# Kernel tuning notes

Hardware: AMD Instinct MI355X
Metric: run time of the kernel (lower is better)

The kernel has to match this reference:

```python
import jax, jax.numpy as jnp
import numpy as np


def setup_inputs() -> dict:
    key = jax.random.key(0)
    ks = jax.random.split(key, 8)
    N, E, F, H = 50000, 400000, 128, 512
    x = jax.random.normal(ks[0], (N, F), dtype=jnp.float32)
    edge_index = jax.random.randint(ks[1], (2, E), 0, N, dtype=jnp.int32)
    W1 = jax.random.normal(ks[2], (H, 2 * F), dtype=jnp.float32) * 0.05
    b1 = jax.random.normal(ks[3], (H,), dtype=jnp.float32) * 0.05
    W2 = jax.random.normal(ks[4], (H, 2 * H), dtype=jnp.float32) * 0.05
    b2 = jax.random.normal(ks[5], (H,), dtype=jnp.float32) * 0.05
    Wo = jax.random.normal(ks[6], (1, H), dtype=jnp.float32) * 0.05
    bo = jax.random.normal(ks[7], (1,), dtype=jnp.float32) * 0.05
    return {"x": x, "edge_index": edge_index, "W1": W1, "b1": b1,
            "W2": W2, "b2": b2, "Wo": Wo, "bo": bo}


def reference(x, edge_index, W1, b1, W2, b2, Wo, bo):
    # GraphSAGE mean aggregation: agg[dst] = mean over incoming edges of h[src]
    N = x.shape[0]
    src = edge_index[0]
    dst = edge_index[1]
    deg = jax.ops.segment_sum(jnp.ones_like(dst, dtype=x.dtype), dst,
                              num_segments=N)
    inv_deg = 1.0 / jnp.maximum(deg, 1.0)  # clamp_min(1.0)

    def agg_mean(h):
        s = jax.ops.segment_sum(h[src], dst, num_segments=N)  # [N, D]
        return s * inv_deg[:, None]

    # Layer 1: concat(self, neigh) -> Linear -> ReLU (dropout = identity, eval)
    n1 = agg_mean(x)
    h1 = jax.nn.relu(jnp.concatenate([x, n1], axis=1) @ W1.T + b1)
    # Layer 2
    n2 = agg_mean(h1)
    h2 = jax.nn.relu(jnp.concatenate([h1, n2], axis=1) @ W2.T + b2)
    # Output head
    logits = h2 @ Wo.T + bo  # [N, 1]
    return jax.nn.sigmoid(logits)
```

## Files before the change

kernel.cpp:

```cpp
#include <hip/hip_runtime.h>
#include <math.h>


typedef __attribute__((ext_vector_type(8))) short bf16x8;
typedef __attribute__((ext_vector_type(4))) float f32x4;

static inline int ceil_div(int a, int b) { return (a + b - 1) / b; }

__device__ inline float bf2f_lo(unsigned u) { return __builtin_bit_cast(float, u << 16); }
__device__ inline float bf2f_hi(unsigned u) { return __builtin_bit_cast(float, u & 0xffff0000u); }
__device__ inline unsigned f2bf(float f) {
    unsigned u = __builtin_bit_cast(unsigned, f);
    u += 0x7fffu + ((u >> 16) & 1u);
    return u >> 16;
}

#define GLOAD_LDS16(gp, lp)                                                   \
    __builtin_amdgcn_global_load_lds(                                         \
        (__attribute__((address_space(1))) void*)(gp),                        \
        (__attribute__((address_space(3))) void*)(lp), 16, 0, 0)


__global__ void cvt3_hist_kernel(const float* __restrict__ a, unsigned short* __restrict__ ao, int na4,
                                 const float* __restrict__ b, unsigned short* __restrict__ bo, int nb4,
                                 const float* __restrict__ c, unsigned short* __restrict__ co, int nc4,
                                 const int* __restrict__ dst, int* __restrict__ deg, int E,
                                 int cvt_blocks) {
    if ((int)blockIdx.x < cvt_blocks) {
        int i = blockIdx.x * 256 + threadIdx.x;
        if (i < na4 + nb4) {
            const float* in; unsigned short* out; int k;
            if (i < na4) { in = a; out = ao; k = i; }
            else         { in = b; out = bo; k = i - na4; }
            float4 v = ((const float4*)in)[k];
            ushort4 o;
            o.x = (unsigned short)f2bf(v.x);
            o.y = (unsigned short)f2bf(v.y);
            o.z = (unsigned short)f2bf(v.z);
            o.w = (unsigned short)f2bf(v.w);
            ((ushort4*)out)[k] = o;
        } else if (i < na4 + nb4 + nc4) {
            int kk = i - na4 - nb4;
            float4 v = ((const float4*)c)[kk];
            ushort4 o;
            o.x = (unsigned short)f2bf(v.x);
            o.y = (unsigned short)f2bf(v.y);
            o.z = (unsigned short)f2bf(v.z);
            o.w = (unsigned short)f2bf(v.w);
            const int cc = kk >> 8;
            const int kq = kk & 255;
            const int t    = kq >> 3;
            const int quad = (kq >> 1) & 3;
            const int j0   = (kq & 1) * 4;
            const int g  = cc >> 6, nt = (cc >> 4) & 3, cl = cc & 15;
            const size_t off =
                ((((size_t)(t * 8 + g) * 4 + nt) * 4 + quad) * 16 + cl) * 8 + j0;
            *(ushort4*)(co + off) = o;
        }
    } else {
        int e = (blockIdx.x - cvt_blocks) * 256 + threadIdx.x;
        if (e < E) atomicAdd(&deg[dst[e]], 1);
    }
}


__global__ __launch_bounds__(256) void chunk_reduce(const int* __restrict__ deg,
                                                    int* __restrict__ partial, int N) {
    int base = blockIdx.x * 1024;
    int s = 0;
    for (int i = threadIdx.x; i < 1024; i += 256) {
        int idx = base + i;
        if (idx < N) s += deg[idx];
    }
    #pragma unroll
    for (int off = 32; off; off >>= 1) s += __shfl_down(s, off);
    __shared__ int ws[4];
    if ((threadIdx.x & 63) == 0) ws[threadIdx.x >> 6] = s;
    __syncthreads();
    if (threadIdx.x == 0) partial[blockIdx.x] = ws[0] + ws[1] + ws[2] + ws[3];
}

__global__ void partial_scan(int* __restrict__ partial, int* __restrict__ rowstartN, int P) {
    int lane = threadIdx.x;
    int v = (lane < P) ? partial[lane] : 0;
    int incl = v;
    #pragma unroll
    for (int off = 1; off < 64; off <<= 1) {
        int t = __shfl_up(incl, off);
        if (lane >= off) incl += t;
    }
    if (lane < P) partial[lane] = incl - v;
    if (lane == 63) *rowstartN = incl;
}

__global__ __launch_bounds__(256) void chunk_scan(const int* __restrict__ deg,
                                                  const int* __restrict__ partial,
                                                  int* __restrict__ rowstart,
                                                  int* __restrict__ cursor, int N) {
    int base = blockIdx.x * 1024 + threadIdx.x * 4;
    int v[4];
    #pragma unroll
    for (int j = 0; j < 4; ++j) {
        int i = base + j;
        v[j] = (i < N) ? deg[i] : 0;
    }
    int mysum = v[0] + v[1] + v[2] + v[3];
    int incl = mysum;
    int lane = threadIdx.x & 63, wave = threadIdx.x >> 6;
    #pragma unroll
    for (int off = 1; off < 64; off <<= 1) {
        int t = __shfl_up(incl, off);
        if (lane >= off) incl += t;
    }
    __shared__ int ws[4];
    if (lane == 63) ws[wave] = incl;
    __syncthreads();
    int run = partial[blockIdx.x] + incl - mysum;
    for (int w = 0; w < wave; ++w) run += ws[w];
    #pragma unroll
    for (int j = 0; j < 4; ++j) {
        int i = base + j;
        if (i < N) { rowstart[i] = run; cursor[i] = run; }
        run += v[j];
    }
}

__global__ void bucket_kernel(const int* __restrict__ src, const int* __restrict__ dst,
                              int* __restrict__ cursor, int* __restrict__ ebuf, int E) {
    int e = blockIdx.x * 256 + threadIdx.x;
    if (e < E) {
        int pos = atomicAdd(&cursor[dst[e]], 1);
        ebuf[pos] = src[e];
    }
}


__global__ void gather_mean_128(const int* __restrict__ rowstart, const int* __restrict__ ebuf,
                                const unsigned* __restrict__ featb, unsigned* __restrict__ outb, int N) {
    int w = (blockIdx.x * blockDim.x + threadIdx.x) >> 6;
    int lane = threadIdx.x & 63;
    if (w >= N) return;
    int e0 = rowstart[w], e1 = rowstart[w + 1];
    float ax = 0.0f, ay = 0.0f;
    for (int i = e0; i < e1; i += 8) {
        int idx[8];
        #pragma unroll
        for (int u = 0; u < 8; ++u) {
            int t = i + u;
            idx[u] = ebuf[t < e1 ? t : e1 - 1];
        }
        unsigned v[8];
        #pragma unroll
        for (int u = 0; u < 8; ++u)
            v[u] = featb[(size_t)idx[u] * 64 + lane];
        #pragma unroll
        for (int u = 0; u < 8; ++u) {
            const float s = (i + u < e1) ? 1.0f : 0.0f;
            ax += s * bf2f_lo(v[u]);
            ay += s * bf2f_hi(v[u]);
        }
    }
    float inv = 1.0f / fmaxf((float)(e1 - e0), 1.0f);
    outb[(size_t)w * 64 + lane] = f2bf(ax * inv) | (f2bf(ay * inv) << 16);
}

__global__ void gather_mean_512(const int* __restrict__ rowstart, const int* __restrict__ ebuf,
                                const unsigned short* __restrict__ featb,
                                unsigned short* __restrict__ outb, int N) {
    int w = (blockIdx.x * blockDim.x + threadIdx.x) >> 6;
    int lane = threadIdx.x & 63;
    if (w >= N) return;
    int e0 = rowstart[w], e1 = rowstart[w + 1];
    float a[8] = {0, 0, 0, 0, 0, 0, 0, 0};
    const uint4* base = (const uint4*)featb;
    for (int i = e0; i < e1; i += 8) {
        int idx[8];
        #pragma unroll
        for (int u = 0; u < 8; ++u) {
            int t = i + u;
            idx[u] = ebuf[t < e1 ? t : e1 - 1];
        }
        uint4 v[8];
        #pragma unroll
        for (int u = 0; u < 8; ++u)
            v[u] = base[(size_t)idx[u] * 64 + lane];
        #pragma unroll
        for (int u = 0; u < 8; ++u) {
            const float s = (i + u < e1) ? 1.0f : 0.0f;
            a[0] += s * bf2f_lo(v[u].x); a[1] += s * bf2f_hi(v[u].x);
            a[2] += s * bf2f_lo(v[u].y); a[3] += s * bf2f_hi(v[u].y);
            a[4] += s * bf2f_lo(v[u].z); a[5] += s * bf2f_hi(v[u].z);
            a[6] += s * bf2f_lo(v[u].w); a[7] += s * bf2f_hi(v[u].w);
        }
    }
    float inv = 1.0f / fmaxf((float)(e1 - e0), 1.0f);
    uint4 o;
    o.x = f2bf(a[0] * inv) | (f2bf(a[1] * inv) << 16);
    o.y = f2bf(a[2] * inv) | (f2bf(a[3] * inv) << 16);
    o.z = f2bf(a[4] * inv) | (f2bf(a[5] * inv) << 16);
    o.w = f2bf(a[6] * inv) | (f2bf(a[7] * inv) << 16);
    ((uint4*)outb)[(size_t)w * 64 + lane] = o;
}

__global__ __launch_bounds__(256) void gemm_mfma(
    const unsigned short* __restrict__ A0,
    const unsigned short* __restrict__ A1,
    const unsigned short* __restrict__ W,
    const float* __restrict__ b,
    unsigned short* __restrict__ outb,
    const float* __restrict__ Wo,
    float* __restrict__ logit,
    int N, int K0, int K1, int C, int mode)
{
    const int nrow = (N + 127) >> 7;
    const int id   = blockIdx.x;
    const int rowb = ((id >> 5) << 3) + (id & 7);
    const int colb = (id >> 3) & 3;
    if (rowb >= nrow) return;

    const int K = K0 + K1;
    const int S = K0;
    __shared__ short As[2][4096];
    __shared__ short Bs[2][4096];

    const int tid  = threadIdx.x;
    const int lane = tid & 63;
    const int wave = tid >> 6;
    const int wm = wave & 1, wn = wave >> 1;
    const int cl = lane & 15, quad = lane >> 4;
    const int row0 = rowb * 128;
    const int col0 = colb * 128;

    const int r = lane >> 2;
    const int j = lane & 3;
    const int trow0 = wave * 32 + r;
    const int trow1 = trow0 + 16;
    const int ar0 = (row0 + trow0 < N) ? row0 + trow0 : N - 1;
    const int ar1 = (row0 + trow1 < N) ? row0 + trow1 : N - 1;
    const size_t aoff0 = (size_t)ar0 * S + j * 8;
    const size_t aoff1 = (size_t)ar1 * S + j * 8;
    const size_t boff0 = (size_t)(col0 + trow0) * K + j * 8;
    const size_t boff1 = (size_t)(col0 + trow1) * K + j * 8;
    const int lds0 = (wave * 32) * 32;
    const int lds1 = (wave * 32 + 16) * 32;

    f32x4 acc[4][4];
    #pragma unroll
    for (int mt = 0; mt < 4; ++mt)
        #pragma unroll
        for (int nt = 0; nt < 4; ++nt)
            acc[mt][nt] = (f32x4){0.f, 0.f, 0.f, 0.f};

    GLOAD_LDS16(A0 + aoff0, &As[0][lds0]);
    GLOAD_LDS16(A0 + aoff1, &As[0][lds1]);
    GLOAD_LDS16(W  + boff0, &Bs[0][lds0]);
    GLOAD_LDS16(W  + boff1, &Bs[0][lds1]);

    const int iters = K >> 5;
    for (int i = 0; i < iters; ++i) {
        const int cur = i & 1;
        __syncthreads();
        if (i + 1 < iters) {
            const int kn = (i + 1) << 5;
            const unsigned short* Ab = (kn < K0) ? (A0 + kn) : (A1 + (kn - K0));
            const unsigned short* Wb = W + kn;
            const int nb = cur ^ 1;
            GLOAD_LDS16(Ab + aoff0, &As[nb][lds0]);
            GLOAD_LDS16(Ab + aoff1, &As[nb][lds1]);
            GLOAD_LDS16(Wb + boff0, &Bs[nb][lds0]);
            GLOAD_LDS16(Wb + boff1, &Bs[nb][lds1]);
        }

        bf16x8 af[4], bfr[4];
        #pragma unroll
        for (int mt = 0; mt < 4; ++mt)
            af[mt] = *(const bf16x8*)&As[cur][(wm * 64 + mt * 16 + cl) * 32 + quad * 8];
        #pragma unroll
        for (int nt = 0; nt < 4; ++nt)
            bfr[nt] = *(const bf16x8*)&Bs[cur][(wn * 64 + nt * 16 + cl) * 32 + quad * 8];

        #pragma unroll
        for (int mt = 0; mt < 4; ++mt)
            #pragma unroll
            for (int nt = 0; nt < 4; ++nt)
                acc[mt][nt] = __builtin_amdgcn_mfma_f32_16x16x32_bf16(
                    af[mt], bfr[nt], acc[mt][nt], 0, 0, 0);
    }

    if (mode == 0) {
        #pragma unroll
        for (int nt = 0; nt < 4; ++nt) {
            const int colx = col0 + wn * 64 + nt * 16 + cl;
            const float bb = b[colx];
            #pragma unroll
            for (int mt = 0; mt < 4; ++mt) {
                #pragma unroll
                for (int rr = 0; rr < 4; ++rr) {
                    int row = row0 + wm * 64 + mt * 16 + quad * 4 + rr;
                    if (row < N)
                        outb[(size_t)row * C + colx] =
                            (unsigned short)f2bf(fmaxf(acc[mt][nt][rr] + bb, 0.0f));
                }
            }
        }
    } else {
        float bv[4], wv2[4];
        #pragma unroll
        for (int nt = 0; nt < 4; ++nt) {
            const int colx = col0 + wn * 64 + nt * 16 + cl;
            bv[nt] = b[colx];
            wv2[nt] = Wo[colx];
        }
        #pragma unroll
        for (int mt = 0; mt < 4; ++mt) {
            #pragma unroll
            for (int rr = 0; rr < 4; ++rr) {
                float s = 0.0f;
                #pragma unroll
                for (int nt = 0; nt < 4; ++nt)
                    s += fmaxf(acc[mt][nt][rr] + bv[nt], 0.0f) * wv2[nt];
                s += __shfl_xor(s, 1);
                s += __shfl_xor(s, 2);
                s += __shfl_xor(s, 4);
                s += __shfl_xor(s, 8);
                int row = row0 + wm * 64 + mt * 16 + quad * 4 + rr;
                if (cl == 0 && row < N) atomicAdd(&logit[row], s);
            }
        }
    }
}


#define STGA(kt) do {                                                          \
    const unsigned short* _p = ((kt) < 16) ? (A0 + ((kt) << 5))                \
                                           : (A1 + (((kt) - 16) << 5));        \
    GLOAD_LDS16(_p + offA, lds + ((kt) % 3) * 8192 + w * 1024);                \
} while (0)

#define LDB(kt) do {                                                           \
    _Pragma("unroll")                                                          \
    for (int _n = 0; _n < 4; ++_n)                                             \
        bq[_n] = *(const bf16x8*)(W +                                          \
            (((size_t)(kt) * 8 + gB) * 4 + _n) * 512 + l * 8);                 \
} while (0)

#define RDA(bf) do {                                                           \
    _Pragma("unroll")                                                          \
    for (int _m = 0; _m < 4; ++_m)                                             \
        af[_m] = *(const bf16x8*)(lds + (bf) * 8192 + aoff + _m * 1024);       \
} while (0)

#define MM16B() do {                                                           \
    _Pragma("unroll")                                                          \
    for (int _m = 0; _m < 4; ++_m)                                             \
        _Pragma("unroll")                                                      \
        for (int _n = 0; _n < 4; ++_n)                                         \
            acc[_m][_n] = __builtin_amdgcn_mfma_f32_16x16x32_bf16(             \
                af[_m], bq[_n], acc[_m][_n], 0, 0, 0);                         \
} while (0)

#define PHASE4(t, stage) do {                                                  \
    __builtin_amdgcn_sched_barrier(0);                                         \
    asm volatile("s_waitcnt vmcnt(5)" ::: "memory");                           \
    __builtin_amdgcn_s_barrier();                                              \
    __builtin_amdgcn_sched_barrier(0);                                         \
    RDA((t) % 3);                                                              \
    if (stage) STGA((t) + 2);                                                  \
    __builtin_amdgcn_s_setprio(1);                                             \
    MM16B();                                                                   \
    __builtin_amdgcn_s_setprio(0);                                             \
    if ((t) + 1 < 32) LDB((t) + 1);                                            \
} while (0)

__global__ __launch_bounds__(512, 4) void gemm2_breg(
    const unsigned short* __restrict__ A0,
    const unsigned short* __restrict__ A1,
    const unsigned short* __restrict__ W,
    const float* __restrict__ b,
    const float* __restrict__ Wo,
    float* __restrict__ logit,
    int N)
{
    __shared__ char lds[24576];

    const int nwg  = ((N + 127) >> 7) * 2;
    const int orig = blockIdx.x;
    const int xcd = orig & 7, lnum = orig >> 3;
    const int q = nwg >> 3, r = nwg & 7;
    const int virt = (xcd < r ? xcd * (q + 1) : r * (q + 1) + (xcd - r) * q) + lnum;
    const int row0 = (virt >> 1) << 7;
    const int col0 = (virt & 1) << 8;

    const int tid = threadIdx.x;
    const int w = tid >> 6, l = tid & 63;
    const int wr = w >> 2, wc = w & 3;
    const int cl = l & 15, quad = l >> 4;
    const int gB = (col0 >> 6) + wc;

    const int c_log = (((l & 3) ^ ((l >> 3) & 3))) * 8;
    int ra = row0 + w * 16 + (l >> 2);
    if (ra > N - 1) ra = N - 1;
    const size_t offA = (size_t)ra * 512 + c_log;

    const int swz  = ((cl >> 1) & 3) << 4;
    const int aoff = (((wr * 64 + cl) * 64) + quad * 16) ^ swz;

    f32x4 acc[4][4];
    #pragma unroll
    for (int mt = 0; mt < 4; ++mt)
        #pragma unroll
        for (int nt = 0; nt < 4; ++nt)
            acc[mt][nt] = (f32x4){0.f, 0.f, 0.f, 0.f};

    bf16x8 af[4], bq[4];

    STGA(0); STGA(1);
    LDB(0);

    #pragma unroll
    for (int t = 0; t < 30; ++t)
        PHASE4(t, 1);
    PHASE4(30, 0);
    PHASE4(31, 0);
    asm volatile("s_waitcnt vmcnt(0)" ::: "memory");

    float bv[4], wv[4];
    #pragma unroll
    for (int nt = 0; nt < 4; ++nt) {
        const int colx = col0 + wc * 64 + nt * 16 + cl;
        bv[nt] = b[colx];
        wv[nt] = Wo[colx];
    }
    #pragma unroll
    for (int mt = 0; mt < 4; ++mt) {
        #pragma unroll
        for (int rr = 0; rr < 4; ++rr) {
            float s = 0.0f;
            #pragma unroll
            for (int nt = 0; nt < 4; ++nt)
                s += fmaxf(acc[mt][nt][rr] + bv[nt], 0.0f) * wv[nt];
            s += __shfl_xor(s, 1);
            s += __shfl_xor(s, 2);
            s += __shfl_xor(s, 4);
            s += __shfl_xor(s, 8);
            const int row = row0 + wr * 64 + mt * 16 + quad * 4 + rr;
            if (cl == 0 && row < N) atomicAdd(&logit[row], s);
        }
    }
}

__global__ void head_kernel(const float* __restrict__ logit, const float* __restrict__ bo,
                            float* __restrict__ out, int N) {
    int i = blockIdx.x * 256 + threadIdx.x;
    if (i < N) out[i] = 1.0f / (1.0f + expf(-(logit[i] + bo[0])));
}

extern "C" void kernel_launch(void* const* d_in, const int* in_sizes, int n_in,
                              void* d_out, int out_size, void* d_ws, size_t ws_size,
                              hipStream_t stream) {
    const float* x  = (const float*)d_in[0];
    const int*   ei = (const int*)d_in[1];
    const float* W1 = (const float*)d_in[2];
    const float* b1 = (const float*)d_in[3];
    const float* W2 = (const float*)d_in[4];
    const float* b2 = (const float*)d_in[5];
    const float* Wo = (const float*)d_in[6];
    const float* bo = (const float*)d_in[7];
    float* out = (float*)d_out;

    const int N = in_sizes[0] / 128;
    const int E = in_sizes[1] / 2;
    const int* src = ei;
    const int* dst = ei + E;

    char* ws = (char*)d_ws;
    size_t off = 0;
    auto alloc = [&](size_t bytes) {
        void* p = ws + off;
        off += (bytes + 255) & ~(size_t)255;
        return p;
    };
    int* deg      = (int*)alloc((size_t)N * 4);
    int* rowstart = (int*)alloc((size_t)(N + 1) * 4);
    int* cursor   = (int*)alloc((size_t)N * 4);
    int* partial  = (int*)alloc((size_t)64 * 4);
    int* ebuf     = (int*)alloc((size_t)E * 4);
    float* logit  = (float*)alloc((size_t)N * 4);
    unsigned short* xb  = (unsigned short*)alloc((size_t)N * 128 * 2);
    unsigned short* W1b = (unsigned short*)alloc((size_t)512 * 256 * 2);
    unsigned short* W2b = (unsigned short*)alloc((size_t)512 * 1024 * 2);
    unsigned short* n1b = (unsigned short*)alloc((size_t)N * 128 * 2);
    unsigned short* h1b = (unsigned short*)alloc((size_t)N * 512 * 2);
    unsigned short* n2b = (unsigned short*)alloc((size_t)N * 512 * 2);
    (void)ws_size; (void)n_in; (void)out_size;

    hipMemsetAsync(deg,   0, (size_t)N * 4, stream);
    hipMemsetAsync(logit, 0, (size_t)N * 4, stream);

    const int na4 = N * 128 / 4, nb4 = 512 * 256 / 4, nc4 = 512 * 1024 / 4;
    const int cvt_blocks  = ceil_div(na4 + nb4 + nc4, 256);
    const int hist_blocks = ceil_div(E, 256);
    cvt3_hist_kernel<<<cvt_blocks + hist_blocks, 256, 0, stream>>>(
        x, xb, na4, W1, W1b, nb4, W2, W2b, nc4, dst, deg, E, cvt_blocks);

    const int P = ceil_div(N, 1024);
    chunk_reduce<<<P, 256, 0, stream>>>(deg, partial, N);
    partial_scan<<<1, 64, 0, stream>>>(partial, rowstart + N, P);
    chunk_scan<<<P, 256, 0, stream>>>(deg, partial, rowstart, cursor, N);
    bucket_kernel<<<ceil_div(E, 256), 256, 0, stream>>>(src, dst, cursor, ebuf, E);

    const int nrow = ceil_div(N, 128);
    const int gblocks = ceil_div(nrow, 8) * 8 * 4;
    gather_mean_128<<<ceil_div(N * 64, 256), 256, 0, stream>>>(rowstart, ebuf,
                                                               (const unsigned*)xb, (unsigned*)n1b, N);
    gemm_mfma<<<gblocks, 256, 0, stream>>>(xb, n1b, W1b, b1, h1b, nullptr, nullptr,
                                           N, 128, 128, 512, 0);

    gather_mean_512<<<ceil_div(N * 64, 256), 256, 0, stream>>>(rowstart, ebuf, h1b, n2b, N);
    const int g2 = ceil_div(N, 128) * 2;
    gemm2_breg<<<g2, 512, 0, stream>>>(h1b, n2b, W2b, b2, Wo, logit, N);

    head_kernel<<<ceil_div(N, 256), 256, 0, stream>>>(logit, bo, out, N);
}
```

Baseline: 317.1 us.

## Make layer-2 GEMM barrier-free with per-wave private A staging and double-buffered B

Replaces the 512-thread, 128x256-tile layer-2 GEMM with a 256-thread, 64x256-tile kernel. In it each wave stages its own full copy of the A tile into a private LDS slice, so the per-step workgroup barrier goes away and only vmcnt waits remain. B fragments are now double-buffered in two register sets to hide global load latency. The cost is that every wave loads A redundantly (4x A traffic and LDS use), there are twice as many workgroups, and register pressure rises under the new launch bounds.

Result: slower. 333.2 us (+5.1%).

```diff
diff --git a/kernel.cpp b/kernel.cpp
--- a/kernel.cpp
+++ b/kernel.cpp
@@ -331,48 +331,44 @@
 }
 
 
-#define STGA(kt) do {                                                          \
+#define STGA2(kt, _bf) do {                                                    \
     const unsigned short* _p = ((kt) < 16) ? (A0 + ((kt) << 5))                \
                                            : (A1 + (((kt) - 16) << 5));        \
-    GLOAD_LDS16(_p + offA, lds + ((kt) % 3) * 8192 + w * 1024);                \
+    GLOAD_LDS16(_p + offA[0], myl + (_bf) * 4096);                             \
+    GLOAD_LDS16(_p + offA[1], myl + (_bf) * 4096 + 1024);                      \
+    GLOAD_LDS16(_p + offA[2], myl + (_bf) * 4096 + 2048);                      \
+    GLOAD_LDS16(_p + offA[3], myl + (_bf) * 4096 + 3072);                      \
 } while (0)
 
-#define LDB(kt) do {                                                           \
+#define LDB2(kt, bqr) do {                                                     \
     _Pragma("unroll")                                                          \
     for (int _n = 0; _n < 4; ++_n)                                             \
-        bq[_n] = *(const bf16x8*)(W +                                          \
+        bqr[_n] = *(const bf16x8*)(W +                                         \
             (((size_t)(kt) * 8 + gB) * 4 + _n) * 512 + l * 8);                 \
 } while (0)
 
-#define RDA(bf) do {                                                           \
+#define RDA2(_bf) do {                                                         \
     _Pragma("unroll")                                                          \
     for (int _m = 0; _m < 4; ++_m)                                             \
-        af[_m] = *(const bf16x8*)(lds + (bf) * 8192 + aoff + _m * 1024);       \
+        af[_m] = *(const bf16x8*)(myl + (_bf) * 4096 + aoff + _m * 1024);      \
 } while (0)
 
-#define MM16B() do {                                                           \
+#define MM16W(bqr) do {                                                        \
     _Pragma("unroll")                                                          \
     for (int _m = 0; _m < 4; ++_m)                                             \
         _Pragma("unroll")                                                      \
         for (int _n = 0; _n < 4; ++_n)                                         \
             acc[_m][_n] = __builtin_amdgcn_mfma_f32_16x16x32_bf16(             \
-                af[_m], bq[_n], acc[_m][_n], 0, 0, 0);                         \
+                af[_m], bqr[_n], acc[_m][_n], 0, 0, 0);                        \
 } while (0)
 
-#define PHASE4(t, stage) do {                                                  \
+#define GATE(nstr) do {                                                        \
     __builtin_amdgcn_sched_barrier(0);                                         \
-    asm volatile("s_waitcnt vmcnt(5)" ::: "memory");                           \
-    __builtin_amdgcn_s_barrier();                                              \
+    asm volatile("s_waitcnt vmcnt(" nstr ")" ::: "memory");                    \
     __builtin_amdgcn_sched_barrier(0);                                         \
-    RDA((t) % 3);                                                              \
-    if (stage) STGA((t) + 2);                                                  \
-    __builtin_amdgcn_s_setprio(1);                                             \
-    MM16B();                                                                   \
-    __builtin_amdgcn_s_setprio(0);                                             \
-    if ((t) + 1 < 32) LDB((t) + 1);                                            \
 } while (0)
 
-__global__ __launch_bounds__(512, 4) void gemm2_breg(
+__global__ __launch_bounds__(256, 3) void gemm2_wnb(
     const unsigned short* __restrict__ A0,
     const unsigned short* __restrict__ A1,
     const unsigned short* __restrict__ W,
@@ -381,29 +377,33 @@
     float* __restrict__ logit,
     int N)
 {
-    __shared__ char lds[24576];
-
-    const int nwg  = ((N + 127) >> 7) * 2;
+    __shared__ char lds[49152];
+
+    const int nwg  = ((N + 63) >> 6) * 2;
     const int orig = blockIdx.x;
     const int xcd = orig & 7, lnum = orig >> 3;
     const int q = nwg >> 3, r = nwg & 7;
     const int virt = (xcd < r ? xcd * (q + 1) : r * (q + 1) + (xcd - r) * q) + lnum;
-    const int row0 = (virt >> 1) << 7;
+    const int row0 = (virt >> 1) << 6;
     const int col0 = (virt & 1) << 8;
 
     const int tid = threadIdx.x;
     const int w = tid >> 6, l = tid & 63;
-    const int wr = w >> 2, wc = w & 3;
     const int cl = l & 15, quad = l >> 4;
-    const int gB = (col0 >> 6) + wc;
+    const int gB = (col0 >> 6) + w;
+    char* myl = lds + w * 12288;
 
     const int c_log = (((l & 3) ^ ((l >> 3) & 3))) * 8;
-    int ra = row0 + w * 16 + (l >> 2);
-    if (ra > N - 1) ra = N - 1;
-    const size_t offA = (size_t)ra * 512 + c_log;
+    size_t offA[4];
+    #pragma unroll
+    for (int i = 0; i < 4; ++i) {
+        int ra = row0 + i * 16 + (l >> 2);
+        if (ra > N - 1) ra = N - 1;
+        offA[i] = (size_t)ra * 512 + c_log;
+    }
 
     const int swz  = ((cl >> 1) & 3) << 4;
-    const int aoff = (((wr * 64 + cl) * 64) + quad * 16) ^ swz;
+    const int aoff = (cl * 64 + quad * 16) ^ swz;
 
     f32x4 acc[4][4];
     #pragma unroll
@@ -412,22 +412,35 @@
         for (int nt = 0; nt < 4; ++nt)
             acc[mt][nt] = (f32x4){0.f, 0.f, 0.f, 0.f};
 
-    bf16x8 af[4], bq[4];
-
-    STGA(0); STGA(1);
-    LDB(0);
-
-    #pragma unroll
-    for (int t = 0; t < 30; ++t)
-        PHASE4(t, 1);
-    PHASE4(30, 0);
-    PHASE4(31, 0);
-    asm volatile("s_waitcnt vmcnt(0)" ::: "memory");
+    bf16x8 af[4], bqA[4], bqB[4];
+
+    STGA2(0, 0); LDB2(0, bqA);
+    STGA2(1, 1); LDB2(1, bqB);
+
+    #pragma unroll
+    for (int t = 0; t < 30; t += 2) {
+        GATE("8");
+        RDA2(t % 3);
+        MM16W(bqA);
+        LDB2(t + 2, bqA);
+        STGA2(t + 2, (t + 2) % 3);
+        GATE("8");
+        RDA2((t + 1) % 3);
+        MM16W(bqB);
+        LDB2(t + 3, bqB);
+        STGA2(t + 3, (t + 3) % 3);
+    }
+    GATE("8");
+    RDA2(0);
+    MM16W(bqA);
+    GATE("0");
+    RDA2(1);
+    MM16W(bqB);
 
     float bv[4], wv[4];
     #pragma unroll
     for (int nt = 0; nt < 4; ++nt) {
-        const int colx = col0 + wc * 64 + nt * 16 + cl;
+        const int colx = col0 + w * 64 + nt * 16 + cl;
         bv[nt] = b[colx];
         wv[nt] = Wo[colx];
     }
@@ -443,7 +456,7 @@
             s += __shfl_xor(s, 2);
             s += __shfl_xor(s, 4);
             s += __shfl_xor(s, 8);
-            const int row = row0 + wr * 64 + mt * 16 + quad * 4 + rr;
+            const int row = row0 + mt * 16 + quad * 4 + rr;
             if (cl == 0 && row < N) atomicAdd(&logit[row], s);
         }
     }
@@ -517,8 +530,8 @@
                                            N, 128, 128, 512, 0);
 
     gather_mean_512<<<ceil_div(N * 64, 256), 256, 0, stream>>>(rowstart, ebuf, h1b, n2b, N);
-    const int g2 = ceil_div(N, 128) * 2;
-    gemm2_breg<<<g2, 512, 0, stream>>>(h1b, n2b, W2b, b2, Wo, logit, N);
+    const int g2 = ceil_div(N, 64) * 2;
+    gemm2_wnb<<<g2, 256, 0, stream>>>(h1b, n2b, W2b, b2, Wo, logit, N);
 
     head_kernel<<<ceil_div(N, 256), 256, 0, stream>>>(logit, bo, out, N);
 }
```

## Port layer-1 GEMM to register-resident B pipeline with pre-swizzled W1

Applied to the files above, without the earlier changes.

Replaces the generic LDS double-buffered layer-1 GEMM with a 512-thread kernel modeled on the layer-2 kernel. It streams A through a triple-buffered LDS ring, loads B directly into registers from a pre-swizzled W1 layout, and uses XCD-aware block remapping. The W1 conversion now writes the MFMA-friendly tiled layout, and B fragments are double-buffered in registers (bqA/bqB) to prefetch two k-steps ahead in both GEMMs. This aims to cut LDS traffic and barrier stalls in GEMM1, at the cost of extra register pressure and a short 8-step pipeline.

New measurement: 316.4 us. No clear change (-0.2%).

```diff
diff --git a/kernel.cpp b/kernel.cpp
--- a/kernel.cpp
+++ b/kernel.cpp
@@ -28,17 +28,31 @@
                                  int cvt_blocks) {
     if ((int)blockIdx.x < cvt_blocks) {
         int i = blockIdx.x * 256 + threadIdx.x;
-        if (i < na4 + nb4) {
-            const float* in; unsigned short* out; int k;
-            if (i < na4) { in = a; out = ao; k = i; }
-            else         { in = b; out = bo; k = i - na4; }
-            float4 v = ((const float4*)in)[k];
+        if (i < na4) {
+            float4 v = ((const float4*)a)[i];
             ushort4 o;
             o.x = (unsigned short)f2bf(v.x);
             o.y = (unsigned short)f2bf(v.y);
             o.z = (unsigned short)f2bf(v.z);
             o.w = (unsigned short)f2bf(v.w);
-            ((ushort4*)out)[k] = o;
+            ((ushort4*)ao)[i] = o;
+        } else if (i < na4 + nb4) {
+            int kk = i - na4;
+            float4 v = ((const float4*)b)[kk];
+            ushort4 o;
+            o.x = (unsigned short)f2bf(v.x);
+            o.y = (unsigned short)f2bf(v.y);
+            o.z = (unsigned short)f2bf(v.z);
+            o.w = (unsigned short)f2bf(v.w);
+            const int cc = kk >> 6;
+            const int kq = kk & 63;
+            const int t    = kq >> 3;
+            const int quad = (kq >> 1) & 3;
+            const int j0   = (kq & 1) * 4;
+            const int g  = cc >> 6, nt = (cc >> 4) & 3, cl = cc & 15;
+            const size_t off =
+                ((((size_t)(t * 8 + g) * 4 + nt) * 4 + quad) * 16 + cl) * 8 + j0;
+            *(ushort4*)(bo + off) = o;
         } else if (i < na4 + nb4 + nc4) {
             int kk = i - na4 - nb4;
             float4 v = ((const float4*)c)[kk];
@@ -202,175 +216,115 @@
     ((uint4*)outb)[(size_t)w * 64 + lane] = o;
 }
 
-__global__ __launch_bounds__(256) void gemm_mfma(
+
+#define STGAg(kt, SPL, STR) do {                                               \
+    const unsigned short* _p = ((kt) < (SPL)) ? (A0 + ((kt) << 5))             \
+                                              : (A1 + (((kt) - (SPL)) << 5));  \
+    GLOAD_LDS16(_p + offA, lds + ((kt) % 3) * 8192 + w * 1024);                \
+} while (0)
+
+#define LDBg(kt, bqr) do {                                                     \
+    _Pragma("unroll")                                                          \
+    for (int _n = 0; _n < 4; ++_n)                                             \
+        bqr[_n] = *(const bf16x8*)(W +                                         \
+            (((size_t)(kt) * 8 + gB) * 4 + _n) * 512 + l * 8);                 \
+} while (0)
+
+#define RDAg(bf) do {                                                         \
+    _Pragma("unroll")                                                          \
+    for (int _m = 0; _m < 4; ++_m)                                             \
+        af[_m] = *(const bf16x8*)(lds + (bf) * 8192 + aoff + _m * 1024);       \
+} while (0)
+
+#define MMg(bqr) do {                                                          \
+    _Pragma("unroll")                                                          \
+    for (int _m = 0; _m < 4; ++_m)                                             \
+        _Pragma("unroll")                                                      \
+        for (int _n = 0; _n < 4; ++_n)                                         \
+            acc[_m][_n] = __builtin_amdgcn_mfma_f32_16x16x32_bf16(             \
+                af[_m], bqr[_n], acc[_m][_n], 0, 0, 0);                        \
+} while (0)
+
+#define PHASEg(t, stg, bqr, gstr, SPL, STR) do {                               \
+    __builtin_amdgcn_sched_barrier(0);                                         \
+    asm volatile("s_waitcnt vmcnt(" gstr ")" ::: "memory");                    \
+    __builtin_amdgcn_s_barrier();                                              \
+    __builtin_amdgcn_sched_barrier(0);                                         \
+    RDAg((t) % 3);                                                             \
+    if (stg) STGAg((t) + 2, SPL, STR);                                         \
+    __builtin_amdgcn_s_setprio(1);                                             \
+    MMg(bqr);                                                                  \
+    __builtin_amdgcn_s_setprio(0);                                             \
+    if (stg) LDBg((t) + 2, bqr);                                               \
+} while (0)
+
+#define BREG_PRELUDE(STR)                                                      \
+    const int nwg  = ((N + 127) >> 7) * 2;                                     \
+    const int orig = blockIdx.x;                                               \
+    const int xcd = orig & 7, lnum = orig >> 3;                                \
+    const int q = nwg >> 3, r = nwg & 7;                                       \
+    const int virt = (xcd < r ? xcd * (q + 1)                                  \
+                              : r * (q + 1) + (xcd - r) * q) + lnum;           \
+    const int row0 = (virt >> 1) << 7;                                         \
+    const int col0 = (virt & 1) << 8;                                          \
+    const int tid = threadIdx.x;                                               \
+    const int w = tid >> 6, l = tid & 63;                                      \
+    const int wr = w >> 2, wc = w & 3;                                         \
+    const int cl = l & 15, quad = l >> 4;                                      \
+    const int gB = (col0 >> 6) + wc;                                           \
+    const int c_log = (((l & 3) ^ ((l >> 3) & 3))) * 8;                        \
+    int ra = row0 + w * 16 + (l >> 2);                                         \
+    if (ra > N - 1) ra = N - 1;                                                \
+    const size_t offA = (size_t)ra * (STR) + c_log;                            \
+    const int swz  = ((cl >> 1) & 3) << 4;                                     \
+    const int aoff = (((wr * 64 + cl) * 64) + quad * 16) ^ swz;                \
+    f32x4 acc[4][4];                                                           \
+    _Pragma("unroll")                                                          \
+    for (int mt = 0; mt < 4; ++mt)                                             \
+        _Pragma("unroll")                                                      \
+        for (int nt = 0; nt < 4; ++nt)                                         \
+            acc[mt][nt] = (f32x4){0.f, 0.f, 0.f, 0.f};                         \
+    bf16x8 af[4], bqA[4], bqB[4];                                              \
+    (void)wr;
+
+__global__ __launch_bounds__(512, 4) void gemm1_breg(
     const unsigned short* __restrict__ A0,
     const unsigned short* __restrict__ A1,
     const unsigned short* __restrict__ W,
     const float* __restrict__ b,
     unsigned short* __restrict__ outb,
-    const float* __restrict__ Wo,
-    float* __restrict__ logit,
-    int N, int K0, int K1, int C, int mode)
+    int N)
 {
-    const int nrow = (N + 127) >> 7;
-    const int id   = blockIdx.x;
-    const int rowb = ((id >> 5) << 3) + (id & 7);
-    const int colb = (id >> 3) & 3;
-    if (rowb >= nrow) return;
-
-    const int K = K0 + K1;
-    const int S = K0;
-    __shared__ short As[2][4096];
-    __shared__ short Bs[2][4096];
-
-    const int tid  = threadIdx.x;
-    const int lane = tid & 63;
-    const int wave = tid >> 6;
-    const int wm = wave & 1, wn = wave >> 1;
-    const int cl = lane & 15, quad = lane >> 4;
-    const int row0 = rowb * 128;
-    const int col0 = colb * 128;
-
-    const int r = lane >> 2;
-    const int j = lane & 3;
-    const int trow0 = wave * 32 + r;
-    const int trow1 = trow0 + 16;
-    const int ar0 = (row0 + trow0 < N) ? row0 + trow0 : N - 1;
-    const int ar1 = (row0 + trow1 < N) ? row0 + trow1 : N - 1;
-    const size_t aoff0 = (size_t)ar0 * S + j * 8;
-    const size_t aoff1 = (size_t)ar1 * S + j * 8;
-    const size_t boff0 = (size_t)(col0 + trow0) * K + j * 8;
-    const size_t boff1 = (size_t)(col0 + trow1) * K + j * 8;
-    const int lds0 = (wave * 32) * 32;
-    const int lds1 = (wave * 32 + 16) * 32;
-
-    f32x4 acc[4][4];
-    #pragma unroll
-    for (int mt = 0; mt < 4; ++mt)
-        #pragma unroll
-        for (int nt = 0; nt < 4; ++nt)
-            acc[mt][nt] = (f32x4){0.f, 0.f, 0.f, 0.f};
-
-    GLOAD_LDS16(A0 + aoff0, &As[0][lds0]);
-    GLOAD_LDS16(A0 + aoff1, &As[0][lds1]);
-    GLOAD_LDS16(W  + boff0, &Bs[0][lds0]);
-    GLOAD_LDS16(W  + boff1, &Bs[0][lds1]);
-
-    const int iters = K >> 5;
-    for (int i = 0; i < iters; ++i) {
-        const int cur = i & 1;
-        __syncthreads();
-        if (i + 1 < iters) {
-            const int kn = (i + 1) << 5;
-            const unsigned short* Ab = (kn < K0) ? (A0 + kn) : (A1 + (kn - K0));
-            const unsigned short* Wb = W + kn;
-            const int nb = cur ^ 1;
-            GLOAD_LDS16(Ab + aoff0, &As[nb][lds0]);
-            GLOAD_LDS16(Ab + aoff1, &As[nb][lds1]);
-            GLOAD_LDS16(Wb + boff0, &Bs[nb][lds0]);
-            GLOAD_LDS16(Wb + boff1, &Bs[nb][lds1]);
-        }
-
-        bf16x8 af[4], bfr[4];
-        #pragma unroll
-        for (int mt = 0; mt < 4; ++mt)
-            af[mt] = *(const bf16x8*)&As[cur][(wm * 64 + mt * 16 + cl) * 32 + quad * 8];
-        #pragma unroll
-        for (int nt = 0; nt < 4; ++nt)
-            bfr[nt] = *(const bf16x8*)&Bs[cur][(wn * 64 + nt * 16 + cl) * 32 + quad * 8];
-
-        #pragma unroll
-        for (int mt = 0; mt < 4; ++mt)
-            #pragma unroll
-            for (int nt = 0; nt < 4; ++nt)
-                acc[mt][nt] = __builtin_amdgcn_mfma_f32_16x16x32_bf16(
-                    af[mt], bfr[nt], acc[mt][nt], 0, 0, 0);
-    }
-
-    if (mode == 0) {
-        #pragma unroll
-        for (int nt = 0; nt < 4; ++nt) {
-            const int colx = col0 + wn * 64 + nt * 16 + cl;
-            const float bb = b[colx];
-            #pragma unroll
-            for (int mt = 0; mt < 4; ++mt) {
-                #pragma unroll
-                for (int rr = 0; rr < 4; ++rr) {
-                    int row = row0 + wm * 64 + mt * 16 + quad * 4 + rr;
-                    if (row < N)
-                        outb[(size_t)row * C + colx] =
-                            (unsigned short)f2bf(fmaxf(acc[mt][nt][rr] + bb, 0.0f));
-                }
-            }
-        }
-    } else {
-        float bv[4], wv2[4];
-        #pragma unroll
-        for (int nt = 0; nt < 4; ++nt) {
-            const int colx = col0 + wn * 64 + nt * 16 + cl;
-            bv[nt] = b[colx];
-            wv2[nt] = Wo[colx];
-        }
+    __shared__ char lds[24576];
+    BREG_PRELUDE(128)
+
+    STGAg(0, 4, 128); LDBg(0, bqA);
+    STGAg(1, 4, 128); LDBg(1, bqB);
+
+    #pragma unroll
+    for (int t = 0; t < 6; t += 2) {
+        PHASEg(t,     1, bqA, "5", 4, 128);
+        PHASEg(t + 1, 1, bqB, "5", 4, 128);
+    }
+    PHASEg(6, 0, bqA, "5", 4, 128);
+    PHASEg(7, 0, bqB, "0", 4, 128);
+
+    #pragma unroll
+    for (int nt = 0; nt < 4; ++nt) {
+        const int colx = col0 + wc * 64 + nt * 16 + cl;
+        const float bb = b[colx];
         #pragma unroll
         for (int mt = 0; mt < 4; ++mt) {
             #pragma unroll
             for (int rr = 0; rr < 4; ++rr) {
-                float s = 0.0f;
-                #pragma unroll
-                for (int nt = 0; nt < 4; ++nt)
-                    s += fmaxf(acc[mt][nt][rr] + bv[nt], 0.0f) * wv2[nt];
-                s += __shfl_xor(s, 1);
-                s += __shfl_xor(s, 2);
-                s += __shfl_xor(s, 4);
-                s += __shfl_xor(s, 8);
-                int row = row0 + wm * 64 + mt * 16 + quad * 4 + rr;
-                if (cl == 0 && row < N) atomicAdd(&logit[row], s);
+                const int row = row0 + wr * 64 + mt * 16 + quad * 4 + rr;
+                if (row < N)
+                    outb[(size_t)row * 512 + colx] =
+                        (unsigned short)f2bf(fmaxf(acc[mt][nt][rr] + bb, 0.0f));
             }
         }
     }
 }
-
-
-#define STGA(kt) do {                                                          \
-    const unsigned short* _p = ((kt) < 16) ? (A0 + ((kt) << 5))                \
-                                           : (A1 + (((kt) - 16) << 5));        \
-    GLOAD_LDS16(_p + offA, lds + ((kt) % 3) * 8192 + w * 1024);                \
-} while (0)
-
-#define LDB(kt) do {                                                           \
-    _Pragma("unroll")                                                          \
-    for (int _n = 0; _n < 4; ++_n)                                             \
-        bq[_n] = *(const bf16x8*)(W +                                          \
-            (((size_t)(kt) * 8 + gB) * 4 + _n) * 512 + l * 8);                 \
-} while (0)
-
-#define RDA(bf) do {                                                           \
-    _Pragma("unroll")                                                          \
-    for (int _m = 0; _m < 4; ++_m)                                             \
-        af[_m] = *(const bf16x8*)(lds + (bf) * 8192 + aoff + _m * 1024);       \
-} while (0)
-
-#define MM16B() do {                                                           \
-    _Pragma("unroll")                                                          \
-    for (int _m = 0; _m < 4; ++_m)                                             \
-        _Pragma("unroll")                                                      \
-        for (int _n = 0; _n < 4; ++_n)                                         \
-            acc[_m][_n] = __builtin_amdgcn_mfma_f32_16x16x32_bf16(             \
-                af[_m], bq[_n], acc[_m][_n], 0, 0, 0);                         \
-} while (0)
-
-#define PHASE4(t, stage) do {                                                  \
-    __builtin_amdgcn_sched_barrier(0);                                         \
-    asm volatile("s_waitcnt vmcnt(5)" ::: "memory");                           \
-    __builtin_amdgcn_s_barrier();                                              \
-    __builtin_amdgcn_sched_barrier(0);                                         \
-    RDA((t) % 3);                                                              \
-    if (stage) STGA((t) + 2);                                                  \
-    __builtin_amdgcn_s_setprio(1);                                             \
-    MM16B();                                                                   \
-    __builtin_amdgcn_s_setprio(0);                                             \
-    if ((t) + 1 < 32) LDB((t) + 1);                                            \
-} while (0)
 
 __global__ __launch_bounds__(512, 4) void gemm2_breg(
     const unsigned short* __restrict__ A0,
@@ -382,47 +336,18 @@
     int N)
 {
     __shared__ char lds[24576];
-
-    const int nwg  = ((N + 127) >> 7) * 2;
-    const int orig = blockIdx.x;
-    const int xcd = orig & 7, lnum = orig >> 3;
-    const int q = nwg >> 3, r = nwg & 7;
-    const int virt = (xcd < r ? xcd * (q + 1) : r * (q + 1) + (xcd - r) * q) + lnum;
-    const int row0 = (virt >> 1) << 7;
-    const int col0 = (virt & 1) << 8;
-
-    const int tid = threadIdx.x;
-    const int w = tid >> 6, l = tid & 63;
-    const int wr = w >> 2, wc = w & 3;
-    const int cl = l & 15, quad = l >> 4;
-    const int gB = (col0 >> 6) + wc;
-
-    const int c_log = (((l & 3) ^ ((l >> 3) & 3))) * 8;
-    int ra = row0 + w * 16 + (l >> 2);
-    if (ra > N - 1) ra = N - 1;
-    const size_t offA = (size_t)ra * 512 + c_log;
-
-    const int swz  = ((cl >> 1) & 3) << 4;
-    const int aoff = (((wr * 64 + cl) * 64) + quad * 16) ^ swz;
-
-    f32x4 acc[4][4];
-    #pragma unroll
-    for (int mt = 0; mt < 4; ++mt)
-        #pragma unroll
-        for (int nt = 0; nt < 4; ++nt)
-            acc[mt][nt] = (f32x4){0.f, 0.f, 0.f, 0.f};
-
-    bf16x8 af[4], bq[4];
-
-    STGA(0); STGA(1);
-    LDB(0);
-
-    #pragma unroll
-    for (int t = 0; t < 30; ++t)
-        PHASE4(t, 1);
-    PHASE4(30, 0);
-    PHASE4(31, 0);
-    asm volatile("s_waitcnt vmcnt(0)" ::: "memory");
+    BREG_PRELUDE(512)
+
+    STGAg(0, 16, 512); LDBg(0, bqA);
+    STGAg(1, 16, 512); LDBg(1, bqB);
+
+    #pragma unroll
+    for (int t = 0; t < 30; t += 2) {
+        PHASEg(t,     1, bqA, "5", 16, 512);
+        PHASEg(t + 1, 1, bqB, "5", 16, 512);
+    }
+    PHASEg(30, 0, bqA, "5", 16, 512);
+    PHASEg(31, 0, bqB, "0", 16, 512);
 
     float bv[4], wv[4];
     #pragma unroll
@@ -509,15 +434,13 @@
     chunk_scan<<<P, 256, 0, stream>>>(deg, partial, rowstart, cursor, N);
     bucket_kernel<<<ceil_div(E, 256), 256, 0, stream>>>(src, dst, cursor, ebuf, E);
 
-    const int nrow = ceil_div(N, 128);
-    const int gblocks = ceil_div(nrow, 8) * 8 * 4;
+    const int g2 = ceil_div(N, 128) * 2;
+
     gather_mean_128<<<ceil_div(N * 64, 256), 256, 0, stream>>>(rowstart, ebuf,
                                                                (const unsigned*)xb, (unsigned*)n1b, N);
-    gemm_mfma<<<gblocks, 256, 0, stream>>>(xb, n1b, W1b, b1, h1b, nullptr, nullptr,
-                                           N, 128, 128, 512, 0);
+    gemm1_breg<<<g2, 512, 0, stream>>>(xb, n1b, W1b, b1, h1b, N);
 
     gather_mean_512<<<ceil_div(N * 64, 256), 256, 0, stream>>>(rowstart, ebuf, h1b, n2b, N);
-    const int g2 = ceil_div(N, 128) * 2;
     gemm2_breg<<<g2, 512, 0, stream>>>(h1b, n2b, W2b, b2, Wo, logit, N);
 
     head_kernel<<<ceil_div(N, 256), 256, 0, stream>>>(logit, bo, out, N);
```
